# Performance work log

Hardware: AMD Instinct MI355X
Metric: run time of the kernel (lower is better)

The kernel has to match this reference:

```python
import jax, jax.numpy as jnp
import numpy as np

NUM_CLASSES = 10
CLS_W, L1_W, GIOU_W = 2.0, 5.0, 2.0


def box_cxcywh_to_xyxy(b):
    cx, cy, w, h = b[..., 0], b[..., 1], b[..., 2], b[..., 3]
    return jnp.stack([cx - w / 2, cy - h / 2, cx + w / 2, cy + h / 2], axis=-1)


def giou_matrix(b1, b2):
    # b1: (B,N,4), b2: (B,M,4) xyxy -> (B,N,M)
    a1 = jnp.clip(b1[..., 2] - b1[..., 0], 0) * jnp.clip(b1[..., 3] - b1[..., 1], 0)
    a2 = jnp.clip(b2[..., 2] - b2[..., 0], 0) * jnp.clip(b2[..., 3] - b2[..., 1], 0)
    lt = jnp.maximum(b1[..., :, None, :2], b2[..., None, :, :2])
    rb = jnp.minimum(b1[..., :, None, 2:], b2[..., None, :, 2:])
    wh = jnp.clip(rb - lt, 0)
    inter = wh[..., 0] * wh[..., 1]
    union = a1[..., :, None] + a2[..., None, :] - inter
    iou = inter / jnp.clip(union, 1e-6)
    lte = jnp.minimum(b1[..., :, None, :2], b2[..., None, :, :2])
    rbe = jnp.maximum(b1[..., :, None, 2:], b2[..., None, :, 2:])
    whe = jnp.clip(rbe - lte, 0)
    enc = whe[..., 0] * whe[..., 1]
    return iou - (enc - union) / jnp.clip(enc, 1e-6)


def giou_elem(b1, b2):
    # b1, b2: (N,4) xyxy, paired -> (N,)
    a1 = jnp.clip(b1[:, 2] - b1[:, 0], 0) * jnp.clip(b1[:, 3] - b1[:, 1], 0)
    a2 = jnp.clip(b2[:, 2] - b2[:, 0], 0) * jnp.clip(b2[:, 3] - b2[:, 1], 0)
    lt = jnp.maximum(b1[:, :2], b2[:, :2])
    rb = jnp.minimum(b1[:, 2:], b2[:, 2:])
    wh = jnp.clip(rb - lt, 0)
    inter = wh[:, 0] * wh[:, 1]
    union = a1 + a2 - inter
    iou = inter / jnp.clip(union, 1e-6)
    lte = jnp.minimum(b1[:, :2], b2[:, :2])
    rbe = jnp.maximum(b1[:, 2:], b2[:, 2:])
    whe = jnp.clip(rbe - lte, 0)
    enc = whe[:, 0] * whe[:, 1]
    return iou - (enc - union) / jnp.clip(enc, 1e-6)


def hungarian(cost):
    # Jonker-Volgenant style shortest-augmenting-path assignment (== scipy.linear_sum_assignment)
    cost = np.asarray(cost, dtype=np.float64)
    transposed = cost.shape[0] > cost.shape[1]
    C = cost.T if transposed else cost
    n, m = C.shape  # n <= m
    u = np.zeros(n + 1)
    v = np.zeros(m + 1)
    p = np.zeros(m + 1, dtype=np.int64)
    colr = np.arange(m + 1)
    for i in range(1, n + 1):
        p[0] = i
        j0 = 0
        minv = np.full(m + 1, np.inf)
        way = np.zeros(m + 1, dtype=np.int64)
        used = np.zeros(m + 1, dtype=bool)
        while True:
            used[j0] = True
            i0 = p[j0]
            unused = colr[1:][~used[1:]]
            cur = C[i0 - 1, unused - 1] - u[i0] - v[unused]
            better = cur < minv[unused]
            bidx = unused[better]
            minv[bidx] = cur[better]
            way[bidx] = j0
            j1 = unused[np.argmin(minv[unused])]
            delta = minv[j1]
            u[p[used]] += delta
            v[used] -= delta
            minv[~used] -= delta
            j0 = j1
            if p[j0] == 0:
                break
        while j0 != 0:
            jn = way[j0]
            p[j0] = p[jn]
            j0 = jn
    rows = p[1:] - 1
    cols = np.arange(m)
    sel = rows >= 0
    r, c = rows[sel], cols[sel]
    if transposed:
        r, c = c, r
    order = np.argsort(r)
    return r[order], c[order]


def compute_matches(pred_logits, pred_boxes, gt_classes, gt_boxes):
    # Batched cost matrices on device, per-sample Hungarian on host (mirrors torch.no_grad matcher).
    B, Q, _ = pred_logits.shape
    G = gt_classes.shape[1]
    prob = jax.nn.softmax(pred_logits, axis=-1)
    cls_idx = jnp.clip(gt_classes, 0, NUM_CLASSES - 1)
    idx = jnp.broadcast_to(cls_idx[:, None, :], (B, Q, G))
    cls_cost = -jnp.take_along_axis(prob, idx, axis=2)                 # (B,Q,G)
    l1_cost = jnp.abs(pred_boxes[:, :, None, :] - gt_boxes[:, None, :, :]).sum(-1)
    g = giou_matrix(box_cxcywh_to_xyxy(pred_boxes), box_cxcywh_to_xyxy(gt_boxes))
    cost = CLS_W * cls_cost + L1_W * l1_cost - GIOU_W * g
    cost_np = np.asarray(jax.device_get(cost))
    valid_np = np.asarray(jax.device_get(gt_classes)) >= 0
    bs, ps, gs = [], [], []
    for bi in range(B):
        vidx = np.nonzero(valid_np[bi])[0]
        if vidx.size == 0:
            continue
        r, c = hungarian(cost_np[bi][:, vidx])
        bs.append(np.full(r.size, bi, dtype=np.int64))
        ps.append(r.astype(np.int64))
        gs.append(vidx[c].astype(np.int64))
    if bs:
        return np.concatenate(bs), np.concatenate(ps), np.concatenate(gs)
    z = np.zeros(0, np.int64)
    return z, z, z


def detection_loss(pred_logits, pred_boxes, gt_boxes, target_cls, b_f, p_f, g_f, n_matched):
    C1 = pred_logits.shape[-1]
    logp = jax.nn.log_softmax(pred_logits, axis=-1).reshape(-1, C1)
    t = target_cls.reshape(-1)
    w = jnp.ones(C1, dtype=pred_logits.dtype).at[-1].set(0.1)
    nll = -jnp.take_along_axis(logp, t[:, None], axis=1)[:, 0]
    wt = w[t]
    cls_loss = (wt * nll).sum() / wt.sum()
    mp = pred_boxes[b_f, p_f]
    mg = gt_boxes[b_f, g_f]
    l1 = jnp.abs(mp - mg).sum()
    gd = giou_elem(box_cxcywh_to_xyxy(mp), box_cxcywh_to_xyxy(mg))
    gl = (1.0 - gd).sum()
    return CLS_W * cls_loss + L1_W * l1 / n_matched + GIOU_W * gl / n_matched


def setup_inputs() -> dict:
    key = jax.random.key(0)
    k1, k2, k3, k4, k5 = jax.random.split(key, 5)
    B, Q, G, C = 64, 900, 100, NUM_CLASSES
    pred_logits = jax.random.normal(k1, (B, Q, C + 1), dtype=jnp.float32)
    pred_boxes = jax.random.uniform(k2, (B, Q, 4), dtype=jnp.float32, minval=0.05, maxval=0.6)
    gt_boxes = jax.random.uniform(k3, (B, G, 4), dtype=jnp.float32, minval=0.05, maxval=0.6)
    cls = jax.random.randint(k4, (B, G), 0, C)
    nvalid = jax.random.randint(k5, (B,), 1, G + 1)
    mask = jnp.arange(G)[None, :] < nvalid[:, None]
    gt_classes = jnp.where(mask, cls, -1).astype(jnp.int32)
    return {"pred_logits": pred_logits, "pred_boxes": pred_boxes,
            "gt_classes": gt_classes, "gt_boxes": gt_boxes}


def reference(pred_logits, pred_boxes, gt_classes, gt_boxes):
    B, Q = pred_logits.shape[:2]
    b_f, p_f, g_f = compute_matches(pred_logits, pred_boxes, gt_classes, gt_boxes)
    gt_np = np.asarray(jax.device_get(gt_classes))
    tc = np.full((B, Q), NUM_CLASSES, dtype=np.int32)
    tc[b_f, p_f] = gt_np[b_f, g_f]
    n_matched = max(int(b_f.size), 1)
    return detection_loss(pred_logits, pred_boxes, gt_boxes, jnp.asarray(tc), b_f, p_f, g_f, n_matched)
```

## Files before the change

### kernel.cpp

```cpp
#include <hip/hip_runtime.h>
#include <hip/hip_bf16.h>
#include <math.h>

#define BB 64
#define QQ 900
#define GG 100
#define NCLS 10
#define CP1 11

#define STRIDE 960
#define KPL 15
#define NT 512
#define NW 8
#define QMASK 255
#define ROUND_CAP 20000

#define NCH 8
#define QCH 128

#define CLS_W 2.0f
#define L1_W 5.0f
#define GIOU_W 2.0f

struct Accum {
  double wnll, wt, l1, gl;
  int nm, counter;
  int pad[6];
};

__global__ __launch_bounds__(256) void cost_kernel(
    const float* __restrict__ logits, const float* __restrict__ pboxes,
    const int* __restrict__ gcls, const float* __restrict__ gboxes,
    float* __restrict__ cost, float4* __restrict__ part, Accum* acc) {
  const int b = blockIdx.y;
  const int chunk = blockIdx.x;
  const int tid = threadIdx.x;
  const int ql = tid & (QCH - 1);
  const int gh = tid >> 7;
  const int q = chunk * QCH + ql;

  if (chunk == 0 && b == 0 && tid == 0) {
    acc->wnll = 0.0; acc->wt = 0.0; acc->l1 = 0.0; acc->gl = 0.0;
    acc->nm = 0; acc->counter = 0;
  }

  __shared__ float s_gb[GG * 4];
  __shared__ int   s_gc[GG];
  __shared__ float s_prob[QCH * 13];
  __shared__ float s_c[GG][QCH + 1];
  __shared__ int   sh_n;

  if (tid == 0) sh_n = 0;
  __syncthreads();

  for (int i = tid; i < GG * 4; i += 256) s_gb[i] = gboxes[b * GG * 4 + i];
  for (int i = tid; i < GG; i += 256) {
    const int v = gcls[b * GG + i];
    s_gc[i] = v;
    if (v >= 0) atomicAdd(&sh_n, 1);
  }

  float pcx = 0.f, pcy = 0.f, pw = 0.f, ph = 0.f;
  if (q < QQ) {
    const float* pb = pboxes + ((size_t)b * QQ + q) * 4;
    pcx = pb[0]; pcy = pb[1]; pw = pb[2]; ph = pb[3];
    if (gh == 0) {
      const float* lg = logits + ((size_t)b * QQ + q) * CP1;
      float l[CP1];
      float mx = -1e30f;
      for (int c = 0; c < CP1; ++c) { l[c] = lg[c]; mx = fmaxf(mx, l[c]); }
      float se = 0.f;
      for (int c = 0; c < CP1; ++c) { l[c] = expf(l[c] - mx); se += l[c]; }
      const float inv = 1.0f / se;
      for (int c = 0; c < NCLS; ++c) s_prob[ql * 13 + c] = l[c] * inv;
    }
  }
  __syncthreads();
  const int sn = sh_n;

  const float px1 = pcx - 0.5f * pw, py1 = pcy - 0.5f * ph;
  const float px2 = pcx + 0.5f * pw, py2 = pcy + 0.5f * ph;
  const float pa = fmaxf(px2 - px1, 0.f) * fmaxf(py2 - py1, 0.f);

  float* crow = cost + ((size_t)b * GG) * STRIDE + q;
  const int g0 = gh * 50;
  const int gend = (g0 + 50 < sn) ? g0 + 50 : sn;
  for (int g = g0; g < gend; ++g) {
    float cv = 3e38f;
    if (q < QQ) {
      int cls = s_gc[g];
      cls = cls < 0 ? 0 : (cls > NCLS - 1 ? NCLS - 1 : cls);
      const float cc = -s_prob[ql * 13 + cls];
      const float gcx = s_gb[g * 4 + 0], gcy = s_gb[g * 4 + 1];
      const float gw  = s_gb[g * 4 + 2], gh2 = s_gb[g * 4 + 3];
      const float l1 = fabsf(pcx - gcx) + fabsf(pcy - gcy) + fabsf(pw - gw) + fabsf(ph - gh2);
      const float gx1 = gcx - 0.5f * gw, gy1 = gcy - 0.5f * gh2;
      const float gx2 = gcx + 0.5f * gw, gy2 = gcy + 0.5f * gh2;
      const float ga = fmaxf(gx2 - gx1, 0.f) * fmaxf(gy2 - gy1, 0.f);
      const float ltx = fmaxf(px1, gx1), lty = fmaxf(py1, gy1);
      const float rbx = fminf(px2, gx2), rby = fminf(py2, gy2);
      const float iw = fmaxf(rbx - ltx, 0.f), ih = fmaxf(rby - lty, 0.f);
      const float inter = iw * ih;
      const float uni = pa + ga - inter;
      const float iou = inter / fmaxf(uni, 1e-6f);
      const float ex1 = fminf(px1, gx1), ey1 = fminf(py1, gy1);
      const float ex2 = fmaxf(px2, gx2), ey2 = fmaxf(py2, gy2);
      const float ew = fmaxf(ex2 - ex1, 0.f), eh = fmaxf(ey2 - ey1, 0.f);
      const float enc = ew * eh;
      const float giou = iou - (enc - uni) / fmaxf(enc, 1e-6f);
      cv = CLS_W * cc + L1_W * l1 - GIOU_W * giou;
      crow[(size_t)g * STRIDE] = cv;
    } else if (q < STRIDE) {
      crow[(size_t)g * STRIDE] = 1e30f;
    }
    s_c[g][ql] = cv;
  }
  __syncthreads();

  if (tid < sn) {
    const int kmax = (chunk == NCH - 1) ? (QQ - (NCH - 1) * QCH) : QCH;
    float m1 = 3e38f, m2 = 3e38f, n1 = 3e38f, n2 = 3e38f;
    int j1 = 0x7FFFFFFF, i1 = 0x7FFFFFFF;
    const int ka = kmax < 64 ? kmax : 64;
    for (int k = 0; k < ka; ++k) {
      const float c = s_c[tid][k];
      if (c < m1) { m2 = m1; m1 = c; j1 = 1 + chunk * QCH + k; }
      else if (c < m2) m2 = c;
    }
    for (int k = 64; k < kmax; ++k) {
      const float c = s_c[tid][k];
      if (c < n1) { n2 = n1; n1 = c; i1 = 1 + chunk * QCH + k; }
      else if (c < n2) n2 = c;
    }
    if (n1 < m1) { m2 = fminf(m1, n2); m1 = n1; j1 = i1; }
    else m2 = fminf(m2, n1);
    part[((size_t)b * NCH + chunk) * QCH + tid] = make_float4(m1, m2, __int_as_float(j1), 0.f);
  }
}

__global__ __launch_bounds__(NT) void jv_kernel(
    const float* __restrict__ logits, const float* __restrict__ pboxes,
    const int* __restrict__ gcls, const float* __restrict__ gboxes,
    const float* __restrict__ cost, const float4* __restrict__ part,
    Accum* acc, float* out) {
  const int b = blockIdx.x;
  const int tid = threadIdx.x;
  const int lane = tid & 63;
  const int w = tid >> 6;

  __shared__ float vl[STRIDE + 2];
  __shared__ int   p[QQ + 1];
  __shared__ unsigned long long way64[STRIDE + 2];
  __shared__ float m1l[GG + 1], m2l[GG + 1];
  __shared__ int   aminl[GG + 1];
  __shared__ int   s_gc[GG];
  __shared__ int   queue[QMASK + 1];
  __shared__ int   sh_n, sh_qtail;
  __shared__ double r0[NW], r1[NW], r2[NW], r3[NW];
  __shared__ int r4[NW];
  __shared__ float s_lse[QQ], s_mx[QQ];

  if (tid == 0) { sh_n = 0; sh_qtail = 0; }
  for (int j = tid; j <= QQ; j += NT) p[j] = 0;
  for (int j = tid; j < STRIDE + 2; j += NT) { vl[j] = 0.f; way64[j] = 0ull; }
  if (tid < GG) s_gc[tid] = gcls[b * GG + tid];
  __syncthreads();
  if (tid < GG && s_gc[tid] >= 0) atomicAdd(&sh_n, 1);
  __syncthreads();
  const int n = sh_n;
  const float* Cb = cost + (size_t)b * GG * STRIDE;

  for (int r = tid; r < n; r += NT) {
    float m1 = 3e38f, m2 = 3e38f;
    int j1 = 0x7FFFFFFF;
#pragma unroll
    for (int ch = 0; ch < NCH; ++ch) {
      const float4 pr = part[((size_t)b * NCH + ch) * QCH + r];
      const float pm1 = pr.x, pm2 = pr.y;
      if (pm1 < m1) { m2 = fminf(m1, pm2); m1 = pm1; j1 = __float_as_int(pr.z); }
      else m2 = fminf(m2, pm1);
    }
    m1l[r] = m1; m2l[r] = m2; aminl[r] = j1;
  }
  __syncthreads();

  if (tid < n) {
    const float regret = m2l[tid] - m1l[tid];
    const unsigned long long key =
        ((unsigned long long)__float_as_uint(regret) << 20) | (unsigned long long)(tid + 1);
    atomicMax(&way64[aminl[tid]], key);
  }
  __syncthreads();
  if (tid < n) {
    const int j1 = aminl[tid];
    if ((int)(way64[j1] & 0xFFFFFu) == tid + 1) {
      p[j1] = tid + 1;
      vl[j1] = m1l[tid] - m2l[tid];
    } else {
      const int t0 = atomicAdd(&sh_qtail, 1);
      queue[t0 & QMASK] = tid + 1;
    }
  }
  __syncthreads();

  if (w == 0) {
    float v[KPL];
#pragma unroll
    for (int k = 0; k < KPL; ++k) v[k] = vl[1 + lane + (k << 6)];
    int head = 0, tail = sh_qtail, rounds = 0;

    float bufA[KPL], bufB[KPL], bufC[KPL];
    int ia = -1, ib = -1, ic = -1;

    auto loadrow = [&](float* buf, int rid) {
      const float* Cr = Cb + (size_t)(rid - 1) * STRIDE + lane;
#pragma unroll
      for (int k = 0; k < KPL; ++k) buf[k] = Cr[k << 6];
    };
    auto do_step = [&](float* rc, int i) {
      float m1 = 3e38f, m2 = 3e38f, n1 = 3e38f, n2 = 3e38f;
      int j1 = 0x7FFFFFFF, i1 = 0x7FFFFFFF;
#pragma unroll
      for (int k = 0; k < 8; ++k) {
        const float c = rc[k] - v[k];
        if (c < m1) { m2 = m1; m1 = c; j1 = 1 + lane + (k << 6); }
        else if (c < m2) m2 = c;
      }
#pragma unroll
      for (int k = 8; k < KPL; ++k) {
        const float c = rc[k] - v[k];
        if (c < n1) { n2 = n1; n1 = c; i1 = 1 + lane + (k << 6); }
        else if (c < n2) n2 = c;
      }
      if (n1 < m1) { m2 = fminf(m1, n2); m1 = n1; j1 = i1; }
      else m2 = fminf(m2, n1);
      for (int m = 1; m < 64; m <<= 1) {
        const float o1 = __shfl_xor(m1, m);
        const float o2 = __shfl_xor(m2, m);
        const int oj = __shfl_xor(j1, m);
        if (o1 < m1) { m2 = fminf(m1, o2); m1 = o1; j1 = oj; }
        else m2 = fminf(m2, o1);
      }
      float d = m2 - m1;
      if (d < 0.f) d = 0.f;
      const int c0 = j1 - 1;
      if ((c0 & 63) == lane) {
        const int kk = c0 >> 6;
        const float ov = v[kk];
        float nv = ov - d;
        if (!(nv < ov)) nv = nextafterf(ov, -3e38f);
        v[kk] = nv;
      }
      const int k0 = p[j1];
      p[j1] = i;
      head++;
      if (k0 > 0) {
        if (lane == 0) queue[tail & QMASK] = k0;
        tail++;
      }
    };

    if (head < tail)     { ia = queue[head & QMASK];       loadrow(bufA, ia); }
    if (head + 1 < tail) { ib = queue[(head + 1) & QMASK]; loadrow(bufB, ib); }
    if (head + 2 < tail) { ic = queue[(head + 2) & QMASK]; loadrow(bufC, ic); }

    while (head < tail && rounds < ROUND_CAP) {
      if (ia < 0) { ia = queue[head & QMASK]; loadrow(bufA, ia); }
      do_step(bufA, ia);
      ia = -1;
      if (head + 2 < tail) { ia = queue[(head + 2) & QMASK]; loadrow(bufA, ia); }
      rounds++;
      if (!(head < tail && rounds < ROUND_CAP)) break;
      if (ib < 0) { ib = queue[head & QMASK]; loadrow(bufB, ib); }
      do_step(bufB, ib);
      ib = -1;
      if (head + 2 < tail) { ib = queue[(head + 2) & QMASK]; loadrow(bufB, ib); }
      rounds++;
      if (!(head < tail && rounds < ROUND_CAP)) break;
      if (ic < 0) { ic = queue[head & QMASK]; loadrow(bufC, ic); }
      do_step(bufC, ic);
      ic = -1;
      if (head + 2 < tail) { ic = queue[(head + 2) & QMASK]; loadrow(bufC, ic); }
      rounds++;
    }
  } else {
    for (int qq = tid - 64; qq < QQ; qq += (NT - 64)) {
      const float* lg = logits + ((size_t)b * QQ + qq) * CP1;
      float l[CP1];
      float mx = -1e30f;
      for (int c = 0; c < CP1; ++c) { l[c] = lg[c]; mx = fmaxf(mx, l[c]); }
      float se = 0.f;
      for (int c = 0; c < CP1; ++c) se += expf(l[c] - mx);
      s_mx[qq] = mx;
      s_lse[qq] = logf(se);
    }
  }
  __syncthreads();

  double wnll = 0.0, wt = 0.0, l1d = 0.0, gld = 0.0;
  int nm = 0;
  for (int q = tid; q < QQ; q += NT) {
    const int idx = b * QQ + q;
    const int g = p[q + 1] - 1;
    const int t = (g >= 0) ? s_gc[g] : NCLS;
    const float lt = logits[(size_t)idx * CP1 + t];
    const float logp = (lt - s_mx[q]) - s_lse[q];
    const float wgt = (t == NCLS) ? 0.1f : 1.0f;
    wnll += (double)(wgt * (-logp));
    wt += (double)wgt;
    if (g >= 0) {
      nm += 1;
      const float* pb = pboxes + (size_t)idx * 4;
      const float* gb = gboxes + ((size_t)b * GG + g) * 4;
      const float pcx = pb[0], pcy = pb[1], pw = pb[2], ph = pb[3];
      const float gcx = gb[0], gcy = gb[1], gw = gb[2], gh = gb[3];
      const float l1 = fabsf(pcx - gcx) + fabsf(pcy - gcy) + fabsf(pw - gw) + fabsf(ph - gh);
      const float px1 = pcx - 0.5f * pw, py1 = pcy - 0.5f * ph;
      const float px2 = pcx + 0.5f * pw, py2 = pcy + 0.5f * ph;
      const float gx1 = gcx - 0.5f * gw, gy1 = gcy - 0.5f * gh;
      const float gx2 = gcx + 0.5f * gw, gy2 = gcy + 0.5f * gh;
      const float pa = fmaxf(px2 - px1, 0.f) * fmaxf(py2 - py1, 0.f);
      const float ga = fmaxf(gx2 - gx1, 0.f) * fmaxf(gy2 - gy1, 0.f);
      const float ltx = fmaxf(px1, gx1), lty = fmaxf(py1, gy1);
      const float rbx = fminf(px2, gx2), rby = fminf(py2, gy2);
      const float iw = fmaxf(rbx - ltx, 0.f), ih = fmaxf(rby - lty, 0.f);
      const float inter = iw * ih;
      const float uni = pa + ga - inter;
      const float iou = inter / fmaxf(uni, 1e-6f);
      const float ex1 = fminf(px1, gx1), ey1 = fminf(py1, gy1);
      const float ex2 = fmaxf(px2, gx2), ey2 = fmaxf(py2, gy2);
      const float ew = fmaxf(ex2 - ex1, 0.f), eh = fmaxf(ey2 - ey1, 0.f);
      const float enc = ew * eh;
      const float giou = iou - (enc - uni) / fmaxf(enc, 1e-6f);
      l1d += (double)l1;
      gld += (double)(1.0f - giou);
    }
  }

  for (int off = 32; off; off >>= 1) {
    wnll += __shfl_down(wnll, off);
    wt   += __shfl_down(wt, off);
    l1d  += __shfl_down(l1d, off);
    gld  += __shfl_down(gld, off);
    nm   += __shfl_down(nm, off);
  }
  if (lane == 0) { r0[w] = wnll; r1[w] = wt; r2[w] = l1d; r3[w] = gld; r4[w] = nm; }
  __syncthreads();
  if (tid == 0) {
    for (int x = 1; x < NW; ++x) { wnll += r0[x]; wt += r1[x]; l1d += r2[x]; gld += r3[x]; nm += r4[x]; }
    atomicAdd(&acc->wnll, wnll);
    atomicAdd(&acc->wt, wt);
    atomicAdd(&acc->l1, l1d);
    atomicAdd(&acc->gl, gld);
    atomicAdd(&acc->nm, nm);
    __threadfence();
    const int ticket = atomicAdd(&acc->counter, 1);
    if (ticket == BB - 1) {
      const double fw = atomicAdd(&acc->wnll, 0.0);
      const double fwt = atomicAdd(&acc->wt, 0.0);
      const double fl1 = atomicAdd(&acc->l1, 0.0);
      const double fgl = atomicAdd(&acc->gl, 0.0);
      int fnm = atomicAdd(&acc->nm, 0);
      if (fnm < 1) fnm = 1;
      const double loss = (double)CLS_W * (fw / fwt) +
                          ((double)L1_W * fl1 + (double)GIOU_W * fgl) / (double)fnm;
      out[0] = (float)loss;
    }
  }
}

extern "C" void kernel_launch(void* const* d_in, const int* in_sizes, int n_in,
                              void* d_out, int out_size, void* d_ws, size_t ws_size,
                              hipStream_t stream) {
  const float* logits = (const float*)d_in[0];
  const float* pboxes = (const float*)d_in[1];
  const int*   gcls   = (const int*)d_in[2];
  const float* gboxes = (const float*)d_in[3];

  char* ws = (char*)d_ws;
  Accum* acc = (Accum*)ws;
  float4* part = (float4*)(ws + 4096);
  float* cost = (float*)(ws + 4096 + (size_t)BB * NCH * QCH * sizeof(float4));

  cost_kernel<<<dim3(NCH, BB), 256, 0, stream>>>(logits, pboxes, gcls, gboxes, cost, part, acc);
  jv_kernel<<<BB, NT, 0, stream>>>(logits, pboxes, gcls, gboxes, cost, part, acc, (float*)d_out);
}
```

Before: 114.6 us.

## Fuse cost-matrix construction into the per-batch assignment kernel

Merges the separate cost kernel and the JV assignment kernel into one kernel with one block per batch. The block loops over query chunks, computing softmax, cost rows and per-row top-2 minima in registers, which removes the intermediate partial-minima buffer and a kernel launch. The log-sum-exp values are now computed during cost construction instead of by idle warps during the JV solve, and the accumulator is zeroed with a memset. The cost is less parallelism for cost construction: 64 blocks instead of 512, with the chunk loop serialized inside each block.

```diff
diff --git a/kernel.cpp b/kernel.cpp
--- a/kernel.cpp
+++ b/kernel.cpp
@@ -28,174 +28,139 @@
   int pad[6];
 };
 
-__global__ __launch_bounds__(256) void cost_kernel(
+__global__ __launch_bounds__(NT) void fused_kernel(
     const float* __restrict__ logits, const float* __restrict__ pboxes,
     const int* __restrict__ gcls, const float* __restrict__ gboxes,
-    float* __restrict__ cost, float4* __restrict__ part, Accum* acc) {
-  const int b = blockIdx.y;
-  const int chunk = blockIdx.x;
+    float* __restrict__ cost, Accum* acc, float* out) {
+  const int b = blockIdx.x;
   const int tid = threadIdx.x;
+  const int lane = tid & 63;
+  const int w = tid >> 6;
   const int ql = tid & (QCH - 1);
-  const int gh = tid >> 7;
-  const int q = chunk * QCH + ql;
-
-  if (chunk == 0 && b == 0 && tid == 0) {
-    acc->wnll = 0.0; acc->wt = 0.0; acc->l1 = 0.0; acc->gl = 0.0;
-    acc->nm = 0; acc->counter = 0;
-  }
+  const int gq = tid >> 7;
 
   __shared__ float s_gb[GG * 4];
   __shared__ int   s_gc[GG];
   __shared__ float s_prob[QCH * 13];
   __shared__ float s_c[GG][QCH + 1];
-  __shared__ int   sh_n;
-
-  if (tid == 0) sh_n = 0;
-  __syncthreads();
-
-  for (int i = tid; i < GG * 4; i += 256) s_gb[i] = gboxes[b * GG * 4 + i];
-  for (int i = tid; i < GG; i += 256) {
-    const int v = gcls[b * GG + i];
-    s_gc[i] = v;
-    if (v >= 0) atomicAdd(&sh_n, 1);
-  }
-
-  float pcx = 0.f, pcy = 0.f, pw = 0.f, ph = 0.f;
-  if (q < QQ) {
-    const float* pb = pboxes + ((size_t)b * QQ + q) * 4;
-    pcx = pb[0]; pcy = pb[1]; pw = pb[2]; ph = pb[3];
-    if (gh == 0) {
-      const float* lg = logits + ((size_t)b * QQ + q) * CP1;
-      float l[CP1];
-      float mx = -1e30f;
-      for (int c = 0; c < CP1; ++c) { l[c] = lg[c]; mx = fmaxf(mx, l[c]); }
-      float se = 0.f;
-      for (int c = 0; c < CP1; ++c) { l[c] = expf(l[c] - mx); se += l[c]; }
-      const float inv = 1.0f / se;
-      for (int c = 0; c < NCLS; ++c) s_prob[ql * 13 + c] = l[c] * inv;
-    }
-  }
-  __syncthreads();
-  const int sn = sh_n;
-
-  const float px1 = pcx - 0.5f * pw, py1 = pcy - 0.5f * ph;
-  const float px2 = pcx + 0.5f * pw, py2 = pcy + 0.5f * ph;
-  const float pa = fmaxf(px2 - px1, 0.f) * fmaxf(py2 - py1, 0.f);
-
-  float* crow = cost + ((size_t)b * GG) * STRIDE + q;
-  const int g0 = gh * 50;
-  const int gend = (g0 + 50 < sn) ? g0 + 50 : sn;
-  for (int g = g0; g < gend; ++g) {
-    float cv = 3e38f;
-    if (q < QQ) {
-      int cls = s_gc[g];
-      cls = cls < 0 ? 0 : (cls > NCLS - 1 ? NCLS - 1 : cls);
-      const float cc = -s_prob[ql * 13 + cls];
-      const float gcx = s_gb[g * 4 + 0], gcy = s_gb[g * 4 + 1];
-      const float gw  = s_gb[g * 4 + 2], gh2 = s_gb[g * 4 + 3];
-      const float l1 = fabsf(pcx - gcx) + fabsf(pcy - gcy) + fabsf(pw - gw) + fabsf(ph - gh2);
-      const float gx1 = gcx - 0.5f * gw, gy1 = gcy - 0.5f * gh2;
-      const float gx2 = gcx + 0.5f * gw, gy2 = gcy + 0.5f * gh2;
-      const float ga = fmaxf(gx2 - gx1, 0.f) * fmaxf(gy2 - gy1, 0.f);
-      const float ltx = fmaxf(px1, gx1), lty = fmaxf(py1, gy1);
-      const float rbx = fminf(px2, gx2), rby = fminf(py2, gy2);
-      const float iw = fmaxf(rbx - ltx, 0.f), ih = fmaxf(rby - lty, 0.f);
-      const float inter = iw * ih;
-      const float uni = pa + ga - inter;
-      const float iou = inter / fmaxf(uni, 1e-6f);
-      const float ex1 = fminf(px1, gx1), ey1 = fminf(py1, gy1);
-      const float ex2 = fmaxf(px2, gx2), ey2 = fmaxf(py2, gy2);
-      const float ew = fmaxf(ex2 - ex1, 0.f), eh = fmaxf(ey2 - ey1, 0.f);
-      const float enc = ew * eh;
-      const float giou = iou - (enc - uni) / fmaxf(enc, 1e-6f);
-      cv = CLS_W * cc + L1_W * l1 - GIOU_W * giou;
-      crow[(size_t)g * STRIDE] = cv;
-    } else if (q < STRIDE) {
-      crow[(size_t)g * STRIDE] = 1e30f;
-    }
-    s_c[g][ql] = cv;
-  }
-  __syncthreads();
-
-  if (tid < sn) {
-    const int kmax = (chunk == NCH - 1) ? (QQ - (NCH - 1) * QCH) : QCH;
-    float m1 = 3e38f, m2 = 3e38f, n1 = 3e38f, n2 = 3e38f;
-    int j1 = 0x7FFFFFFF, i1 = 0x7FFFFFFF;
-    const int ka = kmax < 64 ? kmax : 64;
-    for (int k = 0; k < ka; ++k) {
-      const float c = s_c[tid][k];
-      if (c < m1) { m2 = m1; m1 = c; j1 = 1 + chunk * QCH + k; }
-      else if (c < m2) m2 = c;
-    }
-    for (int k = 64; k < kmax; ++k) {
-      const float c = s_c[tid][k];
-      if (c < n1) { n2 = n1; n1 = c; i1 = 1 + chunk * QCH + k; }
-      else if (c < n2) n2 = c;
-    }
-    if (n1 < m1) { m2 = fminf(m1, n2); m1 = n1; j1 = i1; }
-    else m2 = fminf(m2, n1);
-    part[((size_t)b * NCH + chunk) * QCH + tid] = make_float4(m1, m2, __int_as_float(j1), 0.f);
-  }
-}
-
-__global__ __launch_bounds__(NT) void jv_kernel(
-    const float* __restrict__ logits, const float* __restrict__ pboxes,
-    const int* __restrict__ gcls, const float* __restrict__ gboxes,
-    const float* __restrict__ cost, const float4* __restrict__ part,
-    Accum* acc, float* out) {
-  const int b = blockIdx.x;
-  const int tid = threadIdx.x;
-  const int lane = tid & 63;
-  const int w = tid >> 6;
-
+  __shared__ float s_mx[QQ], s_lse[QQ];
   __shared__ float vl[STRIDE + 2];
   __shared__ int   p[QQ + 1];
   __shared__ unsigned long long way64[STRIDE + 2];
-  __shared__ float m1l[GG + 1], m2l[GG + 1];
-  __shared__ int   aminl[GG + 1];
-  __shared__ int   s_gc[GG];
   __shared__ int   queue[QMASK + 1];
   __shared__ int   sh_n, sh_qtail;
   __shared__ double r0[NW], r1[NW], r2[NW], r3[NW];
   __shared__ int r4[NW];
-  __shared__ float s_lse[QQ], s_mx[QQ];
 
   if (tid == 0) { sh_n = 0; sh_qtail = 0; }
   for (int j = tid; j <= QQ; j += NT) p[j] = 0;
   for (int j = tid; j < STRIDE + 2; j += NT) { vl[j] = 0.f; way64[j] = 0ull; }
+  for (int i = tid; i < GG * 4; i += NT) s_gb[i] = gboxes[b * GG * 4 + i];
   if (tid < GG) s_gc[tid] = gcls[b * GG + tid];
   __syncthreads();
   if (tid < GG && s_gc[tid] >= 0) atomicAdd(&sh_n, 1);
   __syncthreads();
   const int n = sh_n;
-  const float* Cb = cost + (size_t)b * GG * STRIDE;
-
-  for (int r = tid; r < n; r += NT) {
-    float m1 = 3e38f, m2 = 3e38f;
-    int j1 = 0x7FFFFFFF;
-#pragma unroll
-    for (int ch = 0; ch < NCH; ++ch) {
-      const float4 pr = part[((size_t)b * NCH + ch) * QCH + r];
-      const float pm1 = pr.x, pm2 = pr.y;
-      if (pm1 < m1) { m2 = fminf(m1, pm2); m1 = pm1; j1 = __float_as_int(pr.z); }
-      else m2 = fminf(m2, pm1);
-    }
-    m1l[r] = m1; m2l[r] = m2; aminl[r] = j1;
-  }
-  __syncthreads();
+  float* Cb = cost + (size_t)b * GG * STRIDE;
+
+  float rm1 = 3e38f, rm2 = 3e38f;
+  int rj1 = 0x7FFFFFFF;
+  for (int ch = 0; ch < NCH; ++ch) {
+    const int qbase = ch * QCH;
+    if (tid < QCH) {
+      const int q = qbase + tid;
+      if (q < QQ) {
+        const float* lg = logits + ((size_t)b * QQ + q) * CP1;
+        float l[CP1];
+        float mx = -1e30f;
+        for (int c = 0; c < CP1; ++c) { l[c] = lg[c]; mx = fmaxf(mx, l[c]); }
+        float se = 0.f;
+        for (int c = 0; c < CP1; ++c) { l[c] = expf(l[c] - mx); se += l[c]; }
+        const float inv = 1.0f / se;
+        for (int c = 0; c < NCLS; ++c) s_prob[tid * 13 + c] = l[c] * inv;
+        s_mx[q] = mx;
+        s_lse[q] = logf(se);
+      }
+    }
+    __syncthreads();
+
+    const int q = qbase + ql;
+    float pcx = 0.f, pcy = 0.f, pw = 0.f, ph = 0.f;
+    if (q < QQ) {
+      const float* pb = pboxes + ((size_t)b * QQ + q) * 4;
+      pcx = pb[0]; pcy = pb[1]; pw = pb[2]; ph = pb[3];
+    }
+    const float px1 = pcx - 0.5f * pw, py1 = pcy - 0.5f * ph;
+    const float px2 = pcx + 0.5f * pw, py2 = pcy + 0.5f * ph;
+    const float pa = fmaxf(px2 - px1, 0.f) * fmaxf(py2 - py1, 0.f);
+    float* crow = Cb + q;
+    for (int g = gq; g < n; g += 4) {
+      float cv = 3e38f;
+      if (q < QQ) {
+        int cls = s_gc[g];
+        cls = cls < 0 ? 0 : (cls > NCLS - 1 ? NCLS - 1 : cls);
+        const float cc = -s_prob[ql * 13 + cls];
+        const float gcx = s_gb[g * 4 + 0], gcy = s_gb[g * 4 + 1];
+        const float gw  = s_gb[g * 4 + 2], gh2 = s_gb[g * 4 + 3];
+        const float l1 = fabsf(pcx - gcx) + fabsf(pcy - gcy) + fabsf(pw - gw) + fabsf(ph - gh2);
+        const float gx1 = gcx - 0.5f * gw, gy1 = gcy - 0.5f * gh2;
+        const float gx2 = gcx + 0.5f * gw, gy2 = gcy + 0.5f * gh2;
+        const float ga = fmaxf(gx2 - gx1, 0.f) * fmaxf(gy2 - gy1, 0.f);
+        const float ltx = fmaxf(px1, gx1), lty = fmaxf(py1, gy1);
+        const float rbx = fminf(px2, gx2), rby = fminf(py2, gy2);
+        const float iw = fmaxf(rbx - ltx, 0.f), ih = fmaxf(rby - lty, 0.f);
+        const float inter = iw * ih;
+        const float uni = pa + ga - inter;
+        const float iou = inter / fmaxf(uni, 1e-6f);
+        const float ex1 = fminf(px1, gx1), ey1 = fminf(py1, gy1);
+        const float ex2 = fmaxf(px2, gx2), ey2 = fmaxf(py2, gy2);
+        const float ew = fmaxf(ex2 - ex1, 0.f), eh = fmaxf(ey2 - ey1, 0.f);
+        const float enc = ew * eh;
+        const float giou = iou - (enc - uni) / fmaxf(enc, 1e-6f);
+        cv = CLS_W * cc + L1_W * l1 - GIOU_W * giou;
+        crow[(size_t)g * STRIDE] = cv;
+      } else if (q < STRIDE) {
+        crow[(size_t)g * STRIDE] = 1e30f;
+      }
+      s_c[g][ql] = cv;
+    }
+    __syncthreads();
+
+    if (tid < n) {
+      const int kmax = (ch == NCH - 1) ? (QQ - (NCH - 1) * QCH) : QCH;
+      float m1 = 3e38f, m2 = 3e38f, n1 = 3e38f, n2 = 3e38f;
+      int j1 = 0x7FFFFFFF, i1 = 0x7FFFFFFF;
+      const int ka = kmax < 64 ? kmax : 64;
+      for (int k = 0; k < ka; ++k) {
+        const float c = s_c[tid][k];
+        if (c < m1) { m2 = m1; m1 = c; j1 = 1 + qbase + k; }
+        else if (c < m2) m2 = c;
+      }
+      for (int k = 64; k < kmax; ++k) {
+        const float c = s_c[tid][k];
+        if (c < n1) { n2 = n1; n1 = c; i1 = 1 + qbase + k; }
+        else if (c < n2) n2 = c;
+      }
+      if (n1 < m1) { m2 = fminf(m1, n2); m1 = n1; j1 = i1; }
+      else m2 = fminf(m2, n1);
+      if (m1 < rm1) { rm2 = fminf(rm1, m2); rm1 = m1; rj1 = j1; }
+      else rm2 = fminf(rm2, m1);
+    }
+    __syncthreads();
+  }
+  __threadfence_block();
 
   if (tid < n) {
-    const float regret = m2l[tid] - m1l[tid];
+    const float regret = rm2 - rm1;
     const unsigned long long key =
         ((unsigned long long)__float_as_uint(regret) << 20) | (unsigned long long)(tid + 1);
-    atomicMax(&way64[aminl[tid]], key);
+    atomicMax(&way64[rj1], key);
   }
   __syncthreads();
   if (tid < n) {
-    const int j1 = aminl[tid];
-    if ((int)(way64[j1] & 0xFFFFFu) == tid + 1) {
-      p[j1] = tid + 1;
-      vl[j1] = m1l[tid] - m2l[tid];
+    if ((int)(way64[rj1] & 0xFFFFFu) == tid + 1) {
+      p[rj1] = tid + 1;
+      vl[rj1] = rm1 - rm2;
     } else {
       const int t0 = atomicAdd(&sh_qtail, 1);
       queue[t0 & QMASK] = tid + 1;
@@ -282,17 +247,6 @@
       ic = -1;
       if (head + 2 < tail) { ic = queue[(head + 2) & QMASK]; loadrow(bufC, ic); }
       rounds++;
-    }
-  } else {
-    for (int qq = tid - 64; qq < QQ; qq += (NT - 64)) {
-      const float* lg = logits + ((size_t)b * QQ + qq) * CP1;
-      float l[CP1];
-      float mx = -1e30f;
-      for (int c = 0; c < CP1; ++c) { l[c] = lg[c]; mx = fmaxf(mx, l[c]); }
-      float se = 0.f;
-      for (int c = 0; c < CP1; ++c) se += expf(l[c] - mx);
-      s_mx[qq] = mx;
-      s_lse[qq] = logf(se);
     }
   }
   __syncthreads();
@@ -379,9 +333,8 @@
 
   char* ws = (char*)d_ws;
   Accum* acc = (Accum*)ws;
-  float4* part = (float4*)(ws + 4096);
-  float* cost = (float*)(ws + 4096 + (size_t)BB * NCH * QCH * sizeof(float4));
-
-  cost_kernel<<<dim3(NCH, BB), 256, 0, stream>>>(logits, pboxes, gcls, gboxes, cost, part, acc);
-  jv_kernel<<<BB, NT, 0, stream>>>(logits, pboxes, gcls, gboxes, cost, part, acc, (float*)d_out);
+  float* cost = (float*)(ws + 4096);
+
+  hipMemsetAsync(acc, 0, 256, stream);
+  fused_kernel<<<BB, NT, 0, stream>>>(logits, pboxes, gcls, gboxes, cost, acc, (float*)d_out);
 }
```

After: 203.3 us. 1.77x slower.

## Parallelize auction bidding across all warps with atomic conflict resolution

Applied to the files above, without the earlier changes.

Replaces the single-warp sequential auction loop with a batched version: up to eight queued rows bid at once, one per warp, and collisions on the same column are resolved by a regret-keyed atomicMax in shared memory. Losing bidders are pushed back onto the queue. Prices now live in shared memory rather than in registers, and each warp prefetches its next row. The logsumexp precompute moves ahead of the loop so all threads can take part in bidding, and the cost-matrix kernel interleaves GT rows between its two halves. Each round now costs several block-wide barriers, and the batched bidding can change the number of rounds and the tie behaviour compared with the sequential version.

```diff
diff --git a/kernel.cpp b/kernel.cpp
--- a/kernel.cpp
+++ b/kernel.cpp
@@ -83,9 +83,7 @@
   const float pa = fmaxf(px2 - px1, 0.f) * fmaxf(py2 - py1, 0.f);
 
   float* crow = cost + ((size_t)b * GG) * STRIDE + q;
-  const int g0 = gh * 50;
-  const int gend = (g0 + 50 < sn) ? g0 + 50 : sn;
-  for (int g = g0; g < gend; ++g) {
+  for (int g = gh; g < sn; g += 2) {
     float cv = 3e38f;
     if (q < QQ) {
       int cls = s_gc[g];
@@ -155,12 +153,12 @@
   __shared__ int   aminl[GG + 1];
   __shared__ int   s_gc[GG];
   __shared__ int   queue[QMASK + 1];
-  __shared__ int   sh_n, sh_qtail;
+  __shared__ int   sh_n, sh_qtail, sh_head;
   __shared__ double r0[NW], r1[NW], r2[NW], r3[NW];
   __shared__ int r4[NW];
   __shared__ float s_lse[QQ], s_mx[QQ];
 
-  if (tid == 0) { sh_n = 0; sh_qtail = 0; }
+  if (tid == 0) { sh_n = 0; sh_qtail = 0; sh_head = 0; }
   for (int j = tid; j <= QQ; j += NT) p[j] = 0;
   for (int j = tid; j < STRIDE + 2; j += NT) { vl[j] = 0.f; way64[j] = 0ull; }
   if (tid < GG) s_gc[tid] = gcls[b * GG + tid];
@@ -181,6 +179,16 @@
       else m2 = fminf(m2, pm1);
     }
     m1l[r] = m1; m2l[r] = m2; aminl[r] = j1;
+  }
+  for (int qq = tid; qq < QQ; qq += NT) {
+    const float* lg = logits + ((size_t)b * QQ + qq) * CP1;
+    float l[CP1];
+    float mx = -1e30f;
+    for (int c = 0; c < CP1; ++c) { l[c] = lg[c]; mx = fmaxf(mx, l[c]); }
+    float se = 0.f;
+    for (int c = 0; c < CP1; ++c) se += expf(l[c] - mx);
+    s_mx[qq] = mx;
+    s_lse[qq] = logf(se);
   }
   __syncthreads();
 
@@ -203,96 +211,93 @@
   }
   __syncthreads();
 
-  if (w == 0) {
-    float v[KPL];
-#pragma unroll
-    for (int k = 0; k < KPL; ++k) v[k] = vl[1 + lane + (k << 6)];
-    int head = 0, tail = sh_qtail, rounds = 0;
-
-    float bufA[KPL], bufB[KPL], bufC[KPL];
-    int ia = -1, ib = -1, ic = -1;
-
-    auto loadrow = [&](float* buf, int rid) {
-      const float* Cr = Cb + (size_t)(rid - 1) * STRIDE + lane;
-#pragma unroll
-      for (int k = 0; k < KPL; ++k) buf[k] = Cr[k << 6];
-    };
-    auto do_step = [&](float* rc, int i) {
-      float m1 = 3e38f, m2 = 3e38f, n1 = 3e38f, n2 = 3e38f;
-      int j1 = 0x7FFFFFFF, i1 = 0x7FFFFFFF;
-#pragma unroll
-      for (int k = 0; k < 8; ++k) {
-        const float c = rc[k] - v[k];
-        if (c < m1) { m2 = m1; m1 = c; j1 = 1 + lane + (k << 6); }
-        else if (c < m2) m2 = c;
+  {
+    float pf[KPL];
+    int pf_ok = 0, pf_rid = 0;
+    int rounds = 0;
+    while (rounds < ROUND_CAP) {
+      const int head = sh_head, tail = sh_qtail;
+      const int nq = tail - head;
+      if (nq <= 0) break;
+      const int take = nq < NW ? nq : NW;
+      float m1 = 3e38f, m2 = 3e38f;
+      int j1 = 0x7FFFFFFF, rid = 0;
+      if (w < take) {
+        float rc[KPL];
+        if (pf_ok) {
+          rid = pf_rid;
+#pragma unroll
+          for (int k = 0; k < KPL; ++k) rc[k] = pf[k];
+        } else {
+          rid = queue[(head + w) & QMASK];
+          const float* Cr = Cb + (size_t)(rid - 1) * STRIDE + lane;
+#pragma unroll
+          for (int k = 0; k < KPL; ++k) rc[k] = Cr[k << 6];
+        }
+        float n1 = 3e38f, n2 = 3e38f;
+        int i1 = 0x7FFFFFFF;
+#pragma unroll
+        for (int k = 0; k < 8; ++k) {
+          const float c = rc[k] - vl[1 + lane + (k << 6)];
+          if (c < m1) { m2 = m1; m1 = c; j1 = 1 + lane + (k << 6); }
+          else if (c < m2) m2 = c;
+        }
+#pragma unroll
+        for (int k = 8; k < KPL; ++k) {
+          const float c = rc[k] - vl[1 + lane + (k << 6)];
+          if (c < n1) { n2 = n1; n1 = c; i1 = 1 + lane + (k << 6); }
+          else if (c < n2) n2 = c;
+        }
+        if (n1 < m1) { m2 = fminf(m1, n2); m1 = n1; j1 = i1; }
+        else m2 = fminf(m2, n1);
+        for (int m = 1; m < 64; m <<= 1) {
+          const float o1 = __shfl_xor(m1, m);
+          const float o2 = __shfl_xor(m2, m);
+          const int oj = __shfl_xor(j1, m);
+          if (o1 < m1) { m2 = fminf(m1, o2); m1 = o1; j1 = oj; }
+          else m2 = fminf(m2, o1);
+        }
       }
-#pragma unroll
-      for (int k = 8; k < KPL; ++k) {
-        const float c = rc[k] - v[k];
-        if (c < n1) { n2 = n1; n1 = c; i1 = 1 + lane + (k << 6); }
-        else if (c < n2) n2 = c;
+      pf_ok = 0;
+      const int npos = head + take + w;
+      if (npos < tail) {
+        pf_rid = queue[npos & QMASK];
+        const float* Cr = Cb + (size_t)(pf_rid - 1) * STRIDE + lane;
+#pragma unroll
+        for (int k = 0; k < KPL; ++k) pf[k] = Cr[k << 6];
+        pf_ok = 1;
       }
-      if (n1 < m1) { m2 = fminf(m1, n2); m1 = n1; j1 = i1; }
-      else m2 = fminf(m2, n1);
-      for (int m = 1; m < 64; m <<= 1) {
-        const float o1 = __shfl_xor(m1, m);
-        const float o2 = __shfl_xor(m2, m);
-        const int oj = __shfl_xor(j1, m);
-        if (o1 < m1) { m2 = fminf(m1, o2); m1 = o1; j1 = oj; }
-        else m2 = fminf(m2, o1);
+      if (take > 1) {
+        if (w < take && lane == 0) way64[j1] = 0ull;
+        __syncthreads();
+        if (w < take && lane == 0) {
+          float d = m2 - m1;
+          if (d < 0.f) d = 0.f;
+          const unsigned long long key =
+              ((unsigned long long)__float_as_uint(d) << 20) | (unsigned long long)rid;
+          atomicMax(&way64[j1], key);
+        }
+        __syncthreads();
       }
-      float d = m2 - m1;
-      if (d < 0.f) d = 0.f;
-      const int c0 = j1 - 1;
-      if ((c0 & 63) == lane) {
-        const int kk = c0 >> 6;
-        const float ov = v[kk];
-        float nv = ov - d;
-        if (!(nv < ov)) nv = nextafterf(ov, -3e38f);
-        v[kk] = nv;
+      if (w < take && lane == 0) {
+        if (take == 1 || (int)(way64[j1] & 0xFFFFFu) == rid) {
+          float d = m2 - m1;
+          if (d < 0.f) d = 0.f;
+          const float ov = vl[j1];
+          float nv = ov - d;
+          if (!(nv < ov)) nv = nextafterf(ov, -3e38f);
+          vl[j1] = nv;
+          const int k0 = p[j1];
+          p[j1] = rid;
+          if (k0 > 0) { const int t0 = atomicAdd(&sh_qtail, 1); queue[t0 & QMASK] = k0; }
+        } else {
+          const int t0 = atomicAdd(&sh_qtail, 1);
+          queue[t0 & QMASK] = rid;
+        }
       }
-      const int k0 = p[j1];
-      p[j1] = i;
-      head++;
-      if (k0 > 0) {
-        if (lane == 0) queue[tail & QMASK] = k0;
-        tail++;
-      }
-    };
-
-    if (head < tail)     { ia = queue[head & QMASK];       loadrow(bufA, ia); }
-    if (head + 1 < tail) { ib = queue[(head + 1) & QMASK]; loadrow(bufB, ib); }
-    if (head + 2 < tail) { ic = queue[(head + 2) & QMASK]; loadrow(bufC, ic); }
-
-    while (head < tail && rounds < ROUND_CAP) {
-      if (ia < 0) { ia = queue[head & QMASK]; loadrow(bufA, ia); }
-      do_step(bufA, ia);
-      ia = -1;
-      if (head + 2 < tail) { ia = queue[(head + 2) & QMASK]; loadrow(bufA, ia); }
-      rounds++;
-      if (!(head < tail && rounds < ROUND_CAP)) break;
-      if (ib < 0) { ib = queue[head & QMASK]; loadrow(bufB, ib); }
-      do_step(bufB, ib);
-      ib = -1;
-      if (head + 2 < tail) { ib = queue[(head + 2) & QMASK]; loadrow(bufB, ib); }
-      rounds++;
-      if (!(head < tail && rounds < ROUND_CAP)) break;
-      if (ic < 0) { ic = queue[head & QMASK]; loadrow(bufC, ic); }
-      do_step(bufC, ic);
-      ic = -1;
-      if (head + 2 < tail) { ic = queue[(head + 2) & QMASK]; loadrow(bufC, ic); }
-      rounds++;
-    }
-  } else {
-    for (int qq = tid - 64; qq < QQ; qq += (NT - 64)) {
-      const float* lg = logits + ((size_t)b * QQ + qq) * CP1;
-      float l[CP1];
-      float mx = -1e30f;
-      for (int c = 0; c < CP1; ++c) { l[c] = lg[c]; mx = fmaxf(mx, l[c]); }
-      float se = 0.f;
-      for (int c = 0; c < CP1; ++c) se += expf(l[c] - mx);
-      s_mx[qq] = mx;
-      s_lse[qq] = logf(se);
+      if (tid == 0) sh_head = head + take;
+      ++rounds;
+      __syncthreads();
     }
   }
   __syncthreads();
```

Result: faster. 105.0 us (-8.4%).
